# Performance work log

Hardware: AMD Instinct MI355X
Metric: run time of the kernel (lower is better)

## Reference

```python
import jax, jax.numpy as jnp
import numpy as np

SR = 22050
HOP = 512
BINS_PER_OCTAVE = 24
N_OCTAVES = 7
N_BINS = BINS_PER_OCTAVE * N_OCTAVES  # 168
FMIN = 32.7  # center_bins with bins_per_semitone=1 leaves fmin unchanged


def _make_cqt_kernels():
    """Right-aligned (causal) complex CQT kernels, 24 bins/octave, 7 octaves.

    This is the explicit math the stateful SlidingCqt24 C++ routine computes
    incrementally: for each bin k with center freq f_k = fmin * 2^(k/24),
    a Hann-windowed complex exponential of length N_k = ceil(Q*sr/f_k),
    Q = 1/(2^(1/24)-1). Bins are ordered ascending in frequency, matching the
    per-octave np.flip layout of the original forward.
    """
    Q = 1.0 / (2.0 ** (1.0 / BINS_PER_OCTAVE) - 1.0)
    freqs = FMIN * 2.0 ** (np.arange(N_BINS) / BINS_PER_OCTAVE)
    lens = np.ceil(Q * SR / freqs).astype(np.int64)
    n_max = int(lens.max())  # 23014
    kr = np.zeros((N_BINS, n_max), dtype=np.float32)
    ki = np.zeros((N_BINS, n_max), dtype=np.float32)
    for k in range(N_BINS):  # small fixed loop over 168 bins (setup only)
        n = int(lens[k])
        t = np.arange(n)
        win = np.hanning(n)
        c = win * np.exp(2j * np.pi * freqs[k] * t / SR) / n
        kr[k, n_max - n:] = c.real.astype(np.float32)
        ki[k, n_max - n:] = c.imag.astype(np.float32)
    return kr, ki


def setup_inputs() -> dict:
    key = jax.random.key(0)
    audio = jax.random.normal(key, (4, 1, 352768), dtype=jnp.float32)
    kr, ki = _make_cqt_kernels()
    return {
        "audio_waveforms": audio,
        "kern_real": jnp.asarray(kr),
        "kern_imag": jnp.asarray(ki),
    }


def reference(audio_waveforms, kern_real, kern_imag):
    # audio: [B, C, S]; kernels: [K, Nmax]
    n_max = kern_real.shape[1]
    B, C, S = audio_waveforms.shape
    n_blocks = S // HOP  # 689
    # Causal sliding window: block i analyzes the n_max samples ending at
    # sample (i+1)*HOP (left zero-pad for early blocks), matching the
    # block-streaming behavior of the sliding CQT.
    pad = n_max - HOP
    x = jnp.pad(audio_waveforms, ((0, 0), (0, 0), (pad, 0)))
    # Strided frame gather: [n_blocks, Nmax] index table.
    idx = jnp.arange(n_blocks)[:, None] * HOP + jnp.arange(n_max)[None, :]
    frames = x[..., idx]  # [B, C, T, Nmax]
    re = jnp.einsum("bctn,kn->bctk", frames, kern_real)
    im = jnp.einsum("bctn,kn->bctk", frames, kern_imag)
    mag = jnp.sqrt(re * re + im * im)  # [B, C, n_blocks, n_bins]
    return mag
```

## Files before the change

kernel.cpp:

```cpp
#include <hip/hip_runtime.h>
#include <math.h>


namespace {
constexpr int kSR    = 22050;
constexpr int kHop   = 512;
constexpr int kBins  = 168;
constexpr int kT     = 689;
constexpr int kB     = 4;
constexpr int kS     = 352768;
constexpr float kKScale    = 4096.0f;
constexpr float kKScaleInv = 1.0f / 4096.0f;
constexpr int kG16 = 11;
constexpr int kFBB = 88;
constexpr int kAcc = kB * kT * kBins * 2;
constexpr int kTPadB   = 768;
constexpr int kBinPadB = 176;
constexpr int kAccB    = kB * kTPadB * kBinPadB * 2;
}

typedef _Float16 half8 __attribute__((ext_vector_type(8)));
typedef _Float16 half2v __attribute__((ext_vector_type(2)));
typedef float floatx4 __attribute__((ext_vector_type(4)));

struct Jobs {
  int k0[48];
  int lo[48];
  int hi[48];
  int n;
};

struct JobsC {
  int lo16[kG16];
  int cb16[kG16];
  int mlo[3];
  int sm[24];
  int slo[24];
  int shi[24];
  int sbeg[3];
  int scnt[3];
  int ns;
  int totch;
};

__device__ inline void atomAddF(float* p, float v) {
  __hip_atomic_fetch_add(p, v, __ATOMIC_RELAXED, __HIP_MEMORY_SCOPE_AGENT);
}

typedef __attribute__((address_space(3))) unsigned int lds_uint;
typedef __attribute__((address_space(1))) const unsigned int glb_uint;
__device__ __forceinline__ void dma16(const void* g, void* l) {
  __builtin_amdgcn_global_load_lds((glb_uint*)g, (lds_uint*)l, 16, 0, 0);
}

__global__ __launch_bounds__(256) void prep_fused(
    const float* __restrict__ x, const float* __restrict__ kr,
    const float* __restrict__ ki, _Float16* __restrict__ xp,
    _Float16* __restrict__ bp, float* __restrict__ accb,
    const int pad, const int xps, const int nmax,
    const int nbx, const int nbp, const JobsC jt) {
  int bid = blockIdx.x;
  const int tid = threadIdx.x;

  if (bid < nbx) {
    const int octx = xps >> 3;
    const int gid = bid * 256 + tid;
    if (gid >= kB * octx) return;
    const int b = gid / octx;
    const int i = (gid - b * octx) * 8;
    const float* xb = x + (size_t)b * kS - pad;
    half8 h;
    #pragma unroll
    for (int j = 0; j < 8; ++j) {
      const int e = i + j;
      h[j] = (e >= pad && e < pad + kS) ? (_Float16)xb[e] : (_Float16)0.f;
    }
    *(half8*)&xp[(size_t)b * xps + i] = h;
    return;
  }
  bid -= nbx;

  if (bid < nbp) {
    const int chunkid = bid * 4 + (tid >> 6);
    const int lane = tid & 63;
    if (chunkid >= jt.totch) return;
    int g = 0;
    #pragma unroll
    for (int j = 1; j < kG16; ++j)
      if (chunkid >= jt.cb16[j]) g = j;
    const int c = chunkid - jt.cb16[g];
    const int mm = lane & 15;
    const int q  = lane >> 4;
    const int bin  = g * 16 + mm;
    const int col0 = jt.lo16[g] + c * 32 + q * 8;
    const bool binok = (bin < kBins);
    const float* rowr = kr + (size_t)bin * nmax;
    const float* rowi = ki + (size_t)bin * nmax;
    half8 hre, him;
    #pragma unroll
    for (int j = 0; j < 8; ++j) {
      const int col = col0 + j;
      const bool ok = binok && (col < nmax);
      hre[j] = ok ? (_Float16)(rowr[col] * kKScale) : (_Float16)0.f;
      him[j] = ok ? (_Float16)(rowi[col] * kKScale) : (_Float16)0.f;
    }
    _Float16* dst = bp + (size_t)chunkid * 1024 + lane * 8;
    *(half8*)dst = hre;
    *(half8*)(dst + 512) = him;
    return;
  }
  bid -= nbp;

  const int idx = (bid * 256 + tid) * 4;
  if (idx < kAcc)
    *(floatx4*)&accb[idx] = (floatx4){0.f, 0.f, 0.f, 0.f};
}

template <bool PARTIAL>
__global__ __launch_bounds__(256) void cqt_mfma_t(
    const _Float16* __restrict__ bp, const _Float16* __restrict__ xp,
    float* __restrict__ accb, _Float16* __restrict__ part,
    const int xps, const JobsC jt) {
  __shared__ _Float16 lds[2][10240];

  const int sx = blockIdx.y;
  const int fb = blockIdx.x >> 2;
  const int b  = blockIdx.x & 3;
  const int tid  = threadIdx.x;
  const int wave = tid >> 6;
  const int lane = tid & 63;
  const int mm = lane & 15;
  const int q  = lane >> 4;
  const int mac = jt.sm[sx];
  const int g16 = mac * 4 + wave;
  const bool gvalid = (g16 < kG16);
  const int mlo = jt.mlo[mac];
  const int gs = gvalid ? ((jt.lo16[g16] - mlo) >> 5) : 0x7fffffff;
  const int slo = jt.slo[sx];
  const int shi = jt.shi[sx];
  const int fbase = fb * 32;

  const _Float16* xb = xp + (size_t)b * xps;
  int aoff;
  {
    const int tl = wave & 1;
    int row = fbase + tl * 16 + mm;
    if (row > kT - 1) row = kT - 1;
    aoff = row * kHop + q * 8 + ((wave >> 1) * 32);
  }
  const _Float16* bgrp =
      gvalid ? (bp + (size_t)(jt.cb16[g16] - gs) * 1024 + lane * 8) : bp;

  floatx4 accr[2], acci[2];
  #pragma unroll
  for (int tl = 0; tl < 2; ++tl) {
    accr[tl] = (floatx4){0.f, 0.f, 0.f, 0.f};
    acci[tl] = (floatx4){0.f, 0.f, 0.f, 0.f};
  }

  auto stageDMA = [&](int c, int buf) {
    _Float16* L = lds[buf];
    dma16(xb + mlo + c * 32 + aoff, L + wave * 512);
    if (gvalid && c >= gs) {
      const _Float16* bs = bgrp + (size_t)c * 1024;
      #pragma unroll
      for (int cc = 0; cc < 2; ++cc)
        #pragma unroll
        for (int ri = 0; ri < 2; ++ri)
          dma16(bs + cc * 1024 + ri * 512,
                L + 2048 + (wave * 4 + cc * 2 + ri) * 512);
    }
  };

  auto compute = [&](int c, int buf) {
    if (!gvalid || c < gs) return;
    const _Float16* L = lds[buf];
    #pragma unroll
    for (int cc = 0; cc < 2; ++cc) {
      const half8 Bre = *(const half8*)(L + 2048 + (wave * 4 + cc * 2) * 512 + lane * 8);
      const half8 Bim = *(const half8*)(L + 2048 + (wave * 4 + cc * 2 + 1) * 512 + lane * 8);
      #pragma unroll
      for (int tl = 0; tl < 2; ++tl) {
        const half8 A = *(const half8*)(L + (cc * 2 + tl) * 512 + lane * 8);
        accr[tl] = __builtin_amdgcn_mfma_f32_16x16x32_f16(A, Bre, accr[tl], 0, 0, 0);
        acci[tl] = __builtin_amdgcn_mfma_f32_16x16x32_f16(A, Bim, acci[tl], 0, 0, 0);
      }
    }
  };

  stageDMA(slo, 0);
  int buf = 0;
  #pragma unroll 1
  for (int c = slo; c < shi; c += 2) {
    __syncthreads();
    if (c + 2 < shi) stageDMA(c + 2, buf ^ 1);
    compute(c, buf);
    buf ^= 1;
  }

  if (PARTIAL) {
    _Float16* pw = part +
        (((size_t)sx * kFBB + blockIdx.x) * 4 + wave) * 1024 + lane * 16;
    half8 p0, p1;
    #pragma unroll
    for (int r = 0; r < 4; ++r) {
      p0[r * 2]     = (_Float16)accr[0][r];
      p0[r * 2 + 1] = (_Float16)acci[0][r];
      p1[r * 2]     = (_Float16)accr[1][r];
      p1[r * 2 + 1] = (_Float16)acci[1][r];
    }
    *(half8*)pw = p0;
    *(half8*)(pw + 8) = p1;
  } else {
    const int bin = g16 * 16 + mm;
    if (bin < kBins) {
      #pragma unroll
      for (int tl = 0; tl < 2; ++tl) {
        const int tb = fbase + tl * 16 + q * 4;
        #pragma unroll
        for (int r = 0; r < 4; ++r) {
          const int t = tb + r;
          if (t < kT) {
            const size_t o = (((size_t)b * kT + t) * kBins + bin) * 2;
            atomAddF(&accb[o],     accr[tl][r] * kKScaleInv);
            atomAddF(&accb[o + 1], acci[tl][r] * kKScaleInv);
          }
        }
      }
    }
  }
}

__global__ __launch_bounds__(256) void cqt_mag_part(
    const _Float16* __restrict__ part, float* __restrict__ out,
    const JobsC jt) {
  const int fbb = blockIdx.x;
  const int fb = fbb >> 2;
  const int b  = fbb & 3;
  const int wave = threadIdx.x >> 6;
  const int lane = threadIdx.x & 63;
  const int g16 = blockIdx.y * 4 + wave;
  if (g16 >= kG16) return;
  const int mac = g16 >> 2;
  const int w   = g16 & 3;
  const int mm = lane & 15;
  const int q  = lane >> 4;

  float a[16];
  #pragma unroll
  for (int i = 0; i < 16; ++i) a[i] = 0.f;
  const int s0 = jt.sbeg[mac];
  const int s1 = s0 + jt.scnt[mac];
  #pragma unroll 1
  for (int s = s0; s < s1; ++s) {
    const _Float16* p = part +
        (((size_t)s * kFBB + fbb) * 4 + w) * 1024 + lane * 16;
    const half8 v0 = *(const half8*)p;
    const half8 v1 = *(const half8*)(p + 8);
    #pragma unroll
    for (int j = 0; j < 8; ++j) {
      a[j]     += (float)v0[j];
      a[8 + j] += (float)v1[j];
    }
  }
  const int k = g16 * 16 + mm;
  if (k >= kBins) return;
  #pragma unroll
  for (int tl = 0; tl < 2; ++tl) {
    #pragma unroll
    for (int r = 0; r < 4; ++r) {
      const int t = fb * 32 + tl * 16 + q * 4 + r;
      if (t < kT) {
        const float re = a[tl * 8 + r * 2];
        const float im = a[tl * 8 + r * 2 + 1];
        out[((size_t)b * kT + t) * kBins + k] =
            sqrtf(re * re + im * im) * kKScaleInv;
      }
    }
  }
}

__global__ __launch_bounds__(256) void cqt_mag4(
    const float* __restrict__ accb, float* __restrict__ out) {
  const int gid = (blockIdx.x * 256 + threadIdx.x) * 4;
  if (gid >= kB * kT * kBins) return;
  const floatx4 v0 = *(const floatx4*)&accb[gid * 2];
  const floatx4 v1 = *(const floatx4*)&accb[gid * 2 + 4];
  floatx4 o;
  o[0] = sqrtf(v0[0] * v0[0] + v0[1] * v0[1]);
  o[1] = sqrtf(v0[2] * v0[2] + v0[3] * v0[3]);
  o[2] = sqrtf(v1[0] * v1[0] + v1[1] * v1[1]);
  o[3] = sqrtf(v1[2] * v1[2] + v1[3] * v1[3]);
  *(floatx4*)&out[gid] = o;
}

__global__ __launch_bounds__(256) void cqt_mag_final(
    const float* __restrict__ accb, float* __restrict__ out,
    const int tp, const int kp) {
  int gid = blockIdx.x * 256 + threadIdx.x;
  if (gid >= kB * kT * kBins) return;
  const int k = gid % kBins;
  const int r = gid / kBins;
  const int t = r % kT;
  const int b = r / kT;
  const float2 v = ((const float2*)accb)[((size_t)b * tp + t) * kp + k];
  out[gid] = sqrtf(v.x * v.x + v.y * v.y);
}

__global__ __launch_bounds__(256) void prep_x_kernel(
    const float* __restrict__ x, _Float16* __restrict__ xp,
    const int pad, const int xps) {
  const int halfx = xps >> 1;
  int gid = blockIdx.x * 256 + threadIdx.x;
  if (gid >= kB * halfx) return;
  const int b = gid / halfx;
  const int i = (gid - b * halfx) * 2;
  float v0 = 0.f, v1 = 0.f;
  if (i     >= pad && i     < pad + kS) v0 = x[(size_t)b * kS + (i - pad)];
  if (i + 1 >= pad && i + 1 < pad + kS) v1 = x[(size_t)b * kS + (i + 1 - pad)];
  half2v h; h.x = (_Float16)v0; h.y = (_Float16)v1;
  *(half2v*)&xp[(size_t)b * xps + i] = h;
}

__global__ __launch_bounds__(256) void cqt_mfma_kernel(
    const float* __restrict__ kr, const float* __restrict__ ki,
    const _Float16* __restrict__ xp, float* __restrict__ accb,
    const int nmax, const int xps, const Jobs jt) {
  __shared__ _Float16 Bs[2][16][264];
  const int jb = blockIdx.x;
  const int k0   = jt.k0[jb];
  const int n_lo = jt.lo[jb];
  const int n_hi = jt.hi[jb];
  const int b  = blockIdx.z;
  const int fb = blockIdx.y;
  const int tid  = threadIdx.x;
  const int lane = tid & 63;
  const int wave = tid >> 6;
  const int m = lane & 15;
  const int q = lane >> 4;
  const int sbin = tid >> 4;
  const int scol = tid & 15;
  const int gbin = k0 + sbin;
  const bool binok = (gbin < kBins);
  const float* rowr = kr + (size_t)gbin * nmax;
  const float* rowi = ki + (size_t)gbin * nmax;
  const int fbase = fb * 256 + wave * 64;
  const _Float16* ax =
      xp + (size_t)b * xps + (size_t)(fbase + m) * kHop + q * 8;
  floatx4 accr[4], acci[4];
  #pragma unroll
  for (int tl = 0; tl < 4; ++tl) {
    accr[tl] = (floatx4){0.f, 0.f, 0.f, 0.f};
    acci[tl] = (floatx4){0.f, 0.f, 0.f, 0.f};
  }
  for (int n0r = n_lo; n0r < n_hi; n0r += 256) {
    __syncthreads();
    #pragma unroll
    for (int c = 0; c < 16; ++c) {
      const int col = n0r + scol + c * 16;
      const bool ok = binok && (col < nmax);
      const float vr = ok ? rowr[col] : 0.f;
      const float vi = ok ? rowi[col] : 0.f;
      Bs[0][sbin][scol + c * 16] = (_Float16)(vr * kKScale);
      Bs[1][sbin][scol + c * 16] = (_Float16)(vi * kKScale);
    }
    __syncthreads();
    const _Float16* axr = ax + n0r;
    #pragma unroll
    for (int c = 0; c < 8; ++c) {
      const int ko = c * 32 + q * 8;
      const half8 br = *(const half8*)&Bs[0][m][ko];
      const half8 bi = *(const half8*)&Bs[1][m][ko];
      #pragma unroll
      for (int tl = 0; tl < 4; ++tl) {
        const half8 a = *(const half8*)(axr + tl * 16 * kHop + c * 32);
        accr[tl] = __builtin_amdgcn_mfma_f32_16x16x32_f16(a, br, accr[tl], 0, 0, 0);
        acci[tl] = __builtin_amdgcn_mfma_f32_16x16x32_f16(a, bi, acci[tl], 0, 0, 0);
      }
    }
  }
  #pragma unroll
  for (int tl = 0; tl < 4; ++tl) {
    #pragma unroll
    for (int rr = 0; rr < 4; ++rr) {
      const int t = fbase + tl * 16 + q * 4 + rr;
      const size_t o = (((size_t)b * kTPadB + t) * kBinPadB + (k0 + m)) * 2;
      atomAddF(&accb[o],     accr[tl][rr] * kKScaleInv);
      atomAddF(&accb[o + 1], acci[tl][rr] * kKScaleInv);
    }
  }
}

namespace fb32 {
constexpr int TT = 8;
constexpr int KG = 4;
constexpr int kTTiles  = (kT + TT - 1) / TT;
constexpr int kKGroups = kBins / KG;
constexpr int kWaves   = kB * kTTiles * kKGroups;
}

__global__ __launch_bounds__(256) void cqt_mag_kernel(
    const float* __restrict__ x,
    const float* __restrict__ kr,
    const float* __restrict__ ki,
    float* __restrict__ out,
    const int nmax, const int pad) {
  using namespace fb32;
  const int wave = (blockIdx.x << 2) + (threadIdx.x >> 6);
  const int lane = threadIdx.x & 63;
  if (wave >= kWaves) return;
  const int kg    = wave / (kB * kTTiles);
  const int rem   = wave - kg * (kB * kTTiles);
  const int b     = rem / kTTiles;
  const int ttile = rem - b * kTTiles;
  const int k0 = kg * KG;
  const int t0 = ttile * TT;
  const double Q  = 1.0 / (exp2(1.0 / 24.0) - 1.0);
  const double f0 = 32.7 * exp2((double)k0 / 24.0);
  int N = (int)ceil(Q * (double)kSR / f0) + 8;
  int full_start = nmax - N;
  if (full_start < 0) full_start = 0;
  int tbase[TT], lo[TT], t_last;
  { int t = t0 + TT - 1; if (t > kT - 1) t = kT - 1; t_last = t; }
  #pragma unroll
  for (int tt = 0; tt < TT; ++tt) {
    int t = t0 + tt; if (t > kT - 1) t = kT - 1;
    tbase[tt] = b * kS + t * kHop - pad;
    lo[tt]    = pad - t * kHop;
  }
  int head_start = pad - t_last * kHop;
  if (head_start < full_start) head_start = full_start;
  int safe = pad - t0 * kHop;
  if (safe < head_start) safe = head_start;
  int body_start = nmax - ((nmax - safe) & ~63);
  float accr[TT][KG], acci[TT][KG];
  #pragma unroll
  for (int tt = 0; tt < TT; ++tt)
    #pragma unroll
    for (int kk = 0; kk < KG; ++kk) { accr[tt][kk] = 0.f; acci[tt][kk] = 0.f; }
  for (int n = body_start - 64; n > head_start - 64; n -= 64) {
    const int nn = n + lane;
    const bool kok = (nn >= 0);
    float krv[KG], kiv[KG];
    #pragma unroll
    for (int kk = 0; kk < KG; ++kk) {
      krv[kk] = kok ? kr[(k0 + kk) * nmax + nn] : 0.f;
      kiv[kk] = kok ? ki[(k0 + kk) * nmax + nn] : 0.f;
    }
    float a[TT];
    #pragma unroll
    for (int tt = 0; tt < TT; ++tt)
      a[tt] = (nn >= lo[tt]) ? x[tbase[tt] + nn] : 0.f;
    #pragma unroll
    for (int tt = 0; tt < TT; ++tt)
      #pragma unroll
      for (int kk = 0; kk < KG; ++kk) {
        accr[tt][kk] = fmaf(a[tt], krv[kk], accr[tt][kk]);
        acci[tt][kk] = fmaf(a[tt], kiv[kk], acci[tt][kk]);
      }
  }
  for (int n = body_start; n < nmax; n += 64) {
    const int nn = n + lane;
    float krv[KG], kiv[KG];
    #pragma unroll
    for (int kk = 0; kk < KG; ++kk) {
      krv[kk] = kr[(k0 + kk) * nmax + nn];
      kiv[kk] = ki[(k0 + kk) * nmax + nn];
    }
    float a[TT];
    #pragma unroll
    for (int tt = 0; tt < TT; ++tt)
      a[tt] = x[tbase[tt] + nn];
    #pragma unroll
    for (int tt = 0; tt < TT; ++tt)
      #pragma unroll
      for (int kk = 0; kk < KG; ++kk) {
        accr[tt][kk] = fmaf(a[tt], krv[kk], accr[tt][kk]);
        acci[tt][kk] = fmaf(a[tt], kiv[kk], acci[tt][kk]);
      }
  }
  #pragma unroll
  for (int tt = 0; tt < TT; ++tt) {
    #pragma unroll
    for (int kk = 0; kk < KG; ++kk) {
      float r = accr[tt][kk];
      float i = acci[tt][kk];
      #pragma unroll
      for (int s = 32; s > 0; s >>= 1) {
        r += __shfl_xor(r, s, 64);
        i += __shfl_xor(i, s, 64);
      }
      if (lane == 0) {
        const int t = t0 + tt;
        if (t < kT)
          out[(b * kT + t) * kBins + (k0 + kk)] = sqrtf(r * r + i * i);
      }
    }
  }
}

extern "C" void kernel_launch(void* const* d_in, const int* in_sizes, int n_in,
                              void* d_out, int out_size, void* d_ws, size_t ws_size,
                              hipStream_t stream) {
  const float* x  = (const float*)d_in[0];
  const float* kr = (const float*)d_in[1];
  const float* ki = (const float*)d_in[2];
  float* out = (float*)d_out;

  const int nmax = in_sizes[1] / kBins;
  const int pad  = nmax - kHop;

  const int kcap = ((nmax + 255) / 256) * 256;
  const double Q = 1.0 / (exp2(1.0 / 24.0) - 1.0);

  JobsC jc;
  int tot = 0;
  for (int g = 0; g < kG16; ++g) {
    const double f0 = 32.7 * exp2((double)(16 * g) / 24.0);
    const int N = (int)ceil(Q * (double)kSR / f0) + 8;
    int lo = nmax - N;
    if (lo < 0) lo = 0;
    lo &= ~255;
    jc.lo16[g] = lo;
    jc.cb16[g] = tot;
    tot += (kcap - lo) / 32;
  }
  jc.totch = tot;
  int ns = 0;
  for (int m = 0; m < 3; ++m) {
    jc.mlo[m] = jc.lo16[4 * m];
    jc.sbeg[m] = ns;
    const int C = (kcap - jc.mlo[m]) / 32;
    const int nsl = (C + 95) / 96;
    const int len = ((C + nsl - 1) / nsl + 1) & ~1;
    for (int s = 0; s < nsl && ns < 24; ++s) {
      const int lo = s * len;
      if (lo >= C) break;
      int hi = lo + len;
      if (hi > C) hi = C;
      jc.sm[ns] = m; jc.slo[ns] = lo; jc.shi[ns] = hi;
      ++ns;
    }
    jc.scnt[m] = ns - jc.sbeg[m];
  }
  jc.ns = ns;

  const int xpsA = (kT - 1) * kHop + kcap + 256;
  const size_t xpA_bytes = (size_t)kB * xpsA * sizeof(_Float16);
  const size_t bpA_bytes = (size_t)tot * 2048;

  const size_t partP_off   = (xpA_bytes + 511) & ~(size_t)511;
  const size_t partP_bytes = (size_t)ns * kFBB * 4 * 1024 * sizeof(_Float16);
  const size_t bpP_off     = (partP_off + partP_bytes + 511) & ~(size_t)511;
  const size_t ws_P = bpP_off + bpA_bytes;

  const size_t accA_off  = (xpA_bytes + 511) & ~(size_t)511;
  const size_t accA_bytes = (size_t)kAcc * sizeof(float);
  const size_t bpA_off   = (accA_off + accA_bytes + 511) & ~(size_t)511;
  const size_t ws_A = bpA_off + bpA_bytes;

  const int xpsB = (kTPadB - 1) * kHop + kcap + 256;
  const size_t xpB_bytes = (size_t)kB * xpsB * sizeof(_Float16);
  const size_t accB_off  = (xpB_bytes + 511) & ~(size_t)511;
  const size_t accB_bytes = (size_t)kAccB * sizeof(float);
  const size_t ws_B = accB_off + accB_bytes;

  const int nbx = (kB * (xpsA / 8) + 255) / 256;
  const int nbp = (tot + 3) / 4;

  if (ws_size >= ws_P) {
    _Float16* xp   = (_Float16*)d_ws;
    _Float16* part = (_Float16*)((char*)d_ws + partP_off);
    _Float16* bp   = (_Float16*)((char*)d_ws + bpP_off);

    prep_fused<<<nbx + nbp, 256, 0, stream>>>(
        x, kr, ki, xp, bp, (float*)part , pad, xpsA, nmax,
        nbx, nbp, jc);
    {
      dim3 grid(kFBB, ns);
      cqt_mfma_t<true><<<grid, 256, 0, stream>>>(
          bp, xp, nullptr, part, xpsA, jc);
    }
    {
      dim3 grid(kFBB, 3);
      cqt_mag_part<<<grid, 256, 0, stream>>>(part, out, jc);
    }
    return;
  }

  if (ws_size >= ws_A) {
    _Float16* xp = (_Float16*)d_ws;
    float* accb  = (float*)((char*)d_ws + accA_off);
    _Float16* bp = (_Float16*)((char*)d_ws + bpA_off);

    const int nba = (kAcc / 4 + 255) / 256;
    prep_fused<<<nbx + nbp + nba, 256, 0, stream>>>(
        x, kr, ki, xp, bp, accb, pad, xpsA, nmax, nbx, nbp, jc);
    {
      dim3 grid(kFBB, ns);
      cqt_mfma_t<false><<<grid, 256, 0, stream>>>(
          bp, xp, accb, nullptr, xpsA, jc);
    }
    {
      const int total = kB * kT * kBins;
      cqt_mag4<<<(total / 4 + 255) / 256, 256, 0, stream>>>(accb, out);
    }
    return;
  }

  if (ws_size >= ws_B) {
    _Float16* xp = (_Float16*)d_ws;
    float* accb  = (float*)((char*)d_ws + accB_off);
    Jobs jt;
    int nj = 0;
    for (int g = 0; g < 11; ++g) {
      const int gk0 = 16 * g;
      const double f0 = 32.7 * exp2((double)gk0 / 24.0);
      const int N = (int)ceil(Q * (double)kSR / f0) + 8;
      int lo = nmax - N;
      if (lo < 0) lo = 0;
      lo = (lo / 2048) * 2048;
      for (int s = lo; s < kcap && nj < 48; s += 2048) {
        jt.k0[nj] = gk0;
        jt.lo[nj] = s;
        jt.hi[nj] = (s + 2048 < kcap) ? s + 2048 : kcap;
        ++nj;
      }
    }
    jt.n = nj;
    hipMemsetAsync(accb, 0, accB_bytes, stream);
    {
      const int total = kB * (xpsB / 2);
      prep_x_kernel<<<(total + 255) / 256, 256, 0, stream>>>(x, xp, pad, xpsB);
    }
    {
      dim3 grid(nj, kTPadB / 256, kB);
      cqt_mfma_kernel<<<grid, 256, 0, stream>>>(kr, ki, xp, accb, nmax, xpsB, jt);
    }
    {
      const int total = kB * kT * kBins;
      cqt_mag_final<<<(total + 255) / 256, 256, 0, stream>>>(
          accb, out, kTPadB, kBinPadB);
    }
    return;
  }

  {
    const int blocks = fb32::kWaves / 4;
    cqt_mag_kernel<<<blocks, 256, 0, stream>>>(x, kr, ki, out, nmax, pad);
  }
}
```

Measured before the change: 121.4 us.

## Double time-frame tile per block to reuse CQT kernel fragments across 64 frames

Each MFMA block now covers 64 time frames instead of 32, so every wave stages two A fragments and keeps four accumulator pairs. Each loaded kernel (B) fragment is reused across twice as many frames, which halves kernel-coefficient traffic and the block count, and the partial-sum layout and reduction kernel are widened to match. In exchange it uses more LDS and registers per block and launches half as many blocks, which may lower occupancy and parallelism.

```diff
diff --git a/kernel.cpp b/kernel.cpp
--- a/kernel.cpp
+++ b/kernel.cpp
@@ -12,7 +12,7 @@
 constexpr float kKScale    = 4096.0f;
 constexpr float kKScaleInv = 1.0f / 4096.0f;
 constexpr int kG16 = 11;
-constexpr int kFBB = 88;
+constexpr int kFBB = 44;
 constexpr int kAcc = kB * kT * kBins * 2;
 constexpr int kTPadB   = 768;
 constexpr int kBinPadB = 176;
@@ -121,7 +121,7 @@
     const _Float16* __restrict__ bp, const _Float16* __restrict__ xp,
     float* __restrict__ accb, _Float16* __restrict__ part,
     const int xps, const JobsC jt) {
-  __shared__ _Float16 lds[2][10240];
+  __shared__ _Float16 lds[2][12288];
 
   const int sx = blockIdx.y;
   const int fb = blockIdx.x >> 2;
@@ -138,29 +138,35 @@
   const int gs = gvalid ? ((jt.lo16[g16] - mlo) >> 5) : 0x7fffffff;
   const int slo = jt.slo[sx];
   const int shi = jt.shi[sx];
-  const int fbase = fb * 32;
+  const int fbase = fb * 64;
 
   const _Float16* xb = xp + (size_t)b * xps;
-  int aoff;
+  int aoff0, aoff1;
   {
-    const int tl = wave & 1;
-    int row = fbase + tl * 16 + mm;
-    if (row > kT - 1) row = kT - 1;
-    aoff = row * kHop + q * 8 + ((wave >> 1) * 32);
+    const int r0 = wave * 2;
+    int row0 = fbase + (r0 & 3) * 16 + mm;
+    if (row0 > kT - 1) row0 = kT - 1;
+    aoff0 = row0 * kHop + (r0 >> 2) * 32 + q * 8;
+    const int r1 = r0 + 1;
+    int row1 = fbase + (r1 & 3) * 16 + mm;
+    if (row1 > kT - 1) row1 = kT - 1;
+    aoff1 = row1 * kHop + (r1 >> 2) * 32 + q * 8;
   }
   const _Float16* bgrp =
       gvalid ? (bp + (size_t)(jt.cb16[g16] - gs) * 1024 + lane * 8) : bp;
 
-  floatx4 accr[2], acci[2];
-  #pragma unroll
-  for (int tl = 0; tl < 2; ++tl) {
+  floatx4 accr[4], acci[4];
+  #pragma unroll
+  for (int tl = 0; tl < 4; ++tl) {
     accr[tl] = (floatx4){0.f, 0.f, 0.f, 0.f};
     acci[tl] = (floatx4){0.f, 0.f, 0.f, 0.f};
   }
 
   auto stageDMA = [&](int c, int buf) {
     _Float16* L = lds[buf];
-    dma16(xb + mlo + c * 32 + aoff, L + wave * 512);
+    const _Float16* xc = xb + mlo + c * 32;
+    dma16(xc + aoff0, L + (wave * 2) * 512);
+    dma16(xc + aoff1, L + (wave * 2 + 1) * 512);
     if (gvalid && c >= gs) {
       const _Float16* bs = bgrp + (size_t)c * 1024;
       #pragma unroll
@@ -168,7 +174,7 @@
         #pragma unroll
         for (int ri = 0; ri < 2; ++ri)
           dma16(bs + cc * 1024 + ri * 512,
-                L + 2048 + (wave * 4 + cc * 2 + ri) * 512);
+                L + 4096 + (wave * 4 + cc * 2 + ri) * 512);
     }
   };
 
@@ -177,11 +183,11 @@
     const _Float16* L = lds[buf];
     #pragma unroll
     for (int cc = 0; cc < 2; ++cc) {
-      const half8 Bre = *(const half8*)(L + 2048 + (wave * 4 + cc * 2) * 512 + lane * 8);
-      const half8 Bim = *(const half8*)(L + 2048 + (wave * 4 + cc * 2 + 1) * 512 + lane * 8);
-      #pragma unroll
-      for (int tl = 0; tl < 2; ++tl) {
-        const half8 A = *(const half8*)(L + (cc * 2 + tl) * 512 + lane * 8);
+      const half8 Bre = *(const half8*)(L + 4096 + (wave * 4 + cc * 2) * 512 + lane * 8);
+      const half8 Bim = *(const half8*)(L + 4096 + (wave * 4 + cc * 2 + 1) * 512 + lane * 8);
+      #pragma unroll
+      for (int tl = 0; tl < 4; ++tl) {
+        const half8 A = *(const half8*)(L + (cc * 4 + tl) * 512 + lane * 8);
         accr[tl] = __builtin_amdgcn_mfma_f32_16x16x32_f16(A, Bre, accr[tl], 0, 0, 0);
         acci[tl] = __builtin_amdgcn_mfma_f32_16x16x32_f16(A, Bim, acci[tl], 0, 0, 0);
       }
@@ -200,22 +206,22 @@
 
   if (PARTIAL) {
     _Float16* pw = part +
-        (((size_t)sx * kFBB + blockIdx.x) * 4 + wave) * 1024 + lane * 16;
-    half8 p0, p1;
-    #pragma unroll
-    for (int r = 0; r < 4; ++r) {
-      p0[r * 2]     = (_Float16)accr[0][r];
-      p0[r * 2 + 1] = (_Float16)acci[0][r];
-      p1[r * 2]     = (_Float16)accr[1][r];
-      p1[r * 2 + 1] = (_Float16)acci[1][r];
-    }
-    *(half8*)pw = p0;
-    *(half8*)(pw + 8) = p1;
+        (((size_t)sx * kFBB + blockIdx.x) * 4 + wave) * 2048 + lane * 32;
+    #pragma unroll
+    for (int tl = 0; tl < 4; ++tl) {
+      half8 p;
+      #pragma unroll
+      for (int r = 0; r < 4; ++r) {
+        p[r * 2]     = (_Float16)accr[tl][r];
+        p[r * 2 + 1] = (_Float16)acci[tl][r];
+      }
+      *(half8*)(pw + tl * 8) = p;
+    }
   } else {
     const int bin = g16 * 16 + mm;
     if (bin < kBins) {
       #pragma unroll
-      for (int tl = 0; tl < 2; ++tl) {
+      for (int tl = 0; tl < 4; ++tl) {
         const int tb = fbase + tl * 16 + q * 4;
         #pragma unroll
         for (int r = 0; r < 4; ++r) {
@@ -246,30 +252,29 @@
   const int mm = lane & 15;
   const int q  = lane >> 4;
 
-  float a[16];
-  #pragma unroll
-  for (int i = 0; i < 16; ++i) a[i] = 0.f;
+  float a[32];
+  #pragma unroll
+  for (int i = 0; i < 32; ++i) a[i] = 0.f;
   const int s0 = jt.sbeg[mac];
   const int s1 = s0 + jt.scnt[mac];
   #pragma unroll 1
   for (int s = s0; s < s1; ++s) {
     const _Float16* p = part +
-        (((size_t)s * kFBB + fbb) * 4 + w) * 1024 + lane * 16;
-    const half8 v0 = *(const half8*)p;
-    const half8 v1 = *(const half8*)(p + 8);
-    #pragma unroll
-    for (int j = 0; j < 8; ++j) {
-      a[j]     += (float)v0[j];
-      a[8 + j] += (float)v1[j];
+        (((size_t)s * kFBB + fbb) * 4 + w) * 2048 + lane * 32;
+    #pragma unroll
+    for (int tl = 0; tl < 4; ++tl) {
+      const half8 v = *(const half8*)(p + tl * 8);
+      #pragma unroll
+      for (int j = 0; j < 8; ++j) a[tl * 8 + j] += (float)v[j];
     }
   }
   const int k = g16 * 16 + mm;
   if (k >= kBins) return;
   #pragma unroll
-  for (int tl = 0; tl < 2; ++tl) {
+  for (int tl = 0; tl < 4; ++tl) {
     #pragma unroll
     for (int r = 0; r < 4; ++r) {
-      const int t = fb * 32 + tl * 16 + q * 4 + r;
+      const int t = fb * 64 + tl * 16 + q * 4 + r;
       if (t < kT) {
         const float re = a[tl * 8 + r * 2];
         const float im = a[tl * 8 + r * 2 + 1];
@@ -550,7 +555,7 @@
   const size_t bpA_bytes = (size_t)tot * 2048;
 
   const size_t partP_off   = (xpA_bytes + 511) & ~(size_t)511;
-  const size_t partP_bytes = (size_t)ns * kFBB * 4 * 1024 * sizeof(_Float16);
+  const size_t partP_bytes = (size_t)ns * kFBB * 4 * 2048 * sizeof(_Float16);
   const size_t bpP_off     = (partP_off + partP_bytes + 511) & ~(size_t)511;
   const size_t ws_P = bpP_off + bpA_bytes;
 
```

Measured after the change: 119.8 us. No clear change (-1.4%).

## Replace LDS double-buffered DMA staging with direct global loads into MFMA

Applied to the files above, without the earlier changes.

Removes the shared-memory double buffer and the global_load_lds DMA staging in the CQT MFMA kernel. Each wave now loads its A (audio frame) and B (kernel) fragments straight from global memory into registers, with no block barriers. Each wave also starts at its own first nonzero chunk instead of idling through the shared loop. The aim is to cut barrier and LDS overhead and let waves run independently, at the cost of losing cross-wave sharing of A tiles and leaning on the cache for reuse.

```diff
diff --git a/kernel.cpp b/kernel.cpp
--- a/kernel.cpp
+++ b/kernel.cpp
@@ -47,12 +47,6 @@
   __hip_atomic_fetch_add(p, v, __ATOMIC_RELAXED, __HIP_MEMORY_SCOPE_AGENT);
 }
 
-typedef __attribute__((address_space(3))) unsigned int lds_uint;
-typedef __attribute__((address_space(1))) const unsigned int glb_uint;
-__device__ __forceinline__ void dma16(const void* g, void* l) {
-  __builtin_amdgcn_global_load_lds((glb_uint*)g, (lds_uint*)l, 16, 0, 0);
-}
-
 __global__ __launch_bounds__(256) void prep_fused(
     const float* __restrict__ x, const float* __restrict__ kr,
     const float* __restrict__ ki, _Float16* __restrict__ xp,
@@ -121,8 +115,6 @@
     const _Float16* __restrict__ bp, const _Float16* __restrict__ xp,
     float* __restrict__ accb, _Float16* __restrict__ part,
     const int xps, const JobsC jt) {
-  __shared__ _Float16 lds[2][10240];
-
   const int sx = blockIdx.y;
   const int fb = blockIdx.x >> 2;
   const int b  = blockIdx.x & 3;
@@ -135,18 +127,18 @@
   const int g16 = mac * 4 + wave;
   const bool gvalid = (g16 < kG16);
   const int mlo = jt.mlo[mac];
-  const int gs = gvalid ? ((jt.lo16[g16] - mlo) >> 5) : 0x7fffffff;
+  const int gs = gvalid ? ((jt.lo16[g16] - mlo) >> 5) : 0;
   const int slo = jt.slo[sx];
   const int shi = jt.shi[sx];
   const int fbase = fb * 32;
 
-  const _Float16* xb = xp + (size_t)b * xps;
-  int aoff;
-  {
-    const int tl = wave & 1;
+  const _Float16* xb = xp + (size_t)b * xps + mlo;
+  int aoff[2];
+  #pragma unroll
+  for (int tl = 0; tl < 2; ++tl) {
     int row = fbase + tl * 16 + mm;
     if (row > kT - 1) row = kT - 1;
-    aoff = row * kHop + q * 8 + ((wave >> 1) * 32);
+    aoff[tl] = row * kHop + q * 8;
   }
   const _Float16* bgrp =
       gvalid ? (bp + (size_t)(jt.cb16[g16] - gs) * 1024 + lane * 8) : bp;
@@ -158,44 +150,29 @@
     acci[tl] = (floatx4){0.f, 0.f, 0.f, 0.f};
   }
 
-  auto stageDMA = [&](int c, int buf) {
-    _Float16* L = lds[buf];
-    dma16(xb + mlo + c * 32 + aoff, L + wave * 512);
-    if (gvalid && c >= gs) {
-      const _Float16* bs = bgrp + (size_t)c * 1024;
-      #pragma unroll
-      for (int cc = 0; cc < 2; ++cc)
-        #pragma unroll
-        for (int ri = 0; ri < 2; ++ri)
-          dma16(bs + cc * 1024 + ri * 512,
-                L + 2048 + (wave * 4 + cc * 2 + ri) * 512);
-    }
-  };
-
-  auto compute = [&](int c, int buf) {
-    if (!gvalid || c < gs) return;
-    const _Float16* L = lds[buf];
-    #pragma unroll
-    for (int cc = 0; cc < 2; ++cc) {
-      const half8 Bre = *(const half8*)(L + 2048 + (wave * 4 + cc * 2) * 512 + lane * 8);
-      const half8 Bim = *(const half8*)(L + 2048 + (wave * 4 + cc * 2 + 1) * 512 + lane * 8);
-      #pragma unroll
-      for (int tl = 0; tl < 2; ++tl) {
-        const half8 A = *(const half8*)(L + (cc * 2 + tl) * 512 + lane * 8);
-        accr[tl] = __builtin_amdgcn_mfma_f32_16x16x32_f16(A, Bre, accr[tl], 0, 0, 0);
-        acci[tl] = __builtin_amdgcn_mfma_f32_16x16x32_f16(A, Bim, acci[tl], 0, 0, 0);
-      }
-    }
-  };
-
-  stageDMA(slo, 0);
-  int buf = 0;
-  #pragma unroll 1
-  for (int c = slo; c < shi; c += 2) {
-    __syncthreads();
-    if (c + 2 < shi) stageDMA(c + 2, buf ^ 1);
-    compute(c, buf);
-    buf ^= 1;
+  int c0 = slo;
+  if (gvalid) { if (gs > c0) c0 = gs; } else { c0 = shi; }
+
+  #pragma unroll 2
+  for (int c = c0; c < shi; c += 2) {
+    const _Float16* bs = bgrp + (size_t)c * 1024;
+    const half8 Bre0 = *(const half8*)(bs);
+    const half8 Bim0 = *(const half8*)(bs + 512);
+    const half8 Bre1 = *(const half8*)(bs + 1024);
+    const half8 Bim1 = *(const half8*)(bs + 1536);
+    const _Float16* ac = xb + c * 32;
+    const half8 A00 = *(const half8*)(ac + aoff[0]);
+    const half8 A10 = *(const half8*)(ac + aoff[1]);
+    const half8 A01 = *(const half8*)(ac + 32 + aoff[0]);
+    const half8 A11 = *(const half8*)(ac + 32 + aoff[1]);
+    accr[0] = __builtin_amdgcn_mfma_f32_16x16x32_f16(A00, Bre0, accr[0], 0, 0, 0);
+    acci[0] = __builtin_amdgcn_mfma_f32_16x16x32_f16(A00, Bim0, acci[0], 0, 0, 0);
+    accr[1] = __builtin_amdgcn_mfma_f32_16x16x32_f16(A10, Bre0, accr[1], 0, 0, 0);
+    acci[1] = __builtin_amdgcn_mfma_f32_16x16x32_f16(A10, Bim0, acci[1], 0, 0, 0);
+    accr[0] = __builtin_amdgcn_mfma_f32_16x16x32_f16(A01, Bre1, accr[0], 0, 0, 0);
+    acci[0] = __builtin_amdgcn_mfma_f32_16x16x32_f16(A01, Bim1, acci[0], 0, 0, 0);
+    accr[1] = __builtin_amdgcn_mfma_f32_16x16x32_f16(A11, Bre1, accr[1], 0, 0, 0);
+    acci[1] = __builtin_amdgcn_mfma_f32_16x16x32_f16(A11, Bim1, acci[1], 0, 0, 0);
   }
 
   if (PARTIAL) {
@@ -213,7 +190,7 @@
     *(half8*)(pw + 8) = p1;
   } else {
     const int bin = g16 * 16 + mm;
-    if (bin < kBins) {
+    if (gvalid && bin < kBins) {
       #pragma unroll
       for (int tl = 0; tl < 2; ++tl) {
         const int tb = fbase + tl * 16 + q * 4;
```

Result: slower. 148.0 us (+21.8%).
